# Performance work log

Measured on AMD Instinct MI355X. Metric: run time of the kernel, lower is better.

The kernel has to match this reference:

```python
import jax, jax.numpy as jnp
import numpy as np

EPS = 1.1920929e-07  # torch RMSNorm default eps = float32 finfo eps

def rms_norm(x, w):
    return x * jax.lax.rsqrt(jnp.mean(x * x, axis=-1, keepdims=True) + EPS) * w

def setup_inputs() -> dict:
    key = jax.random.key(0)
    ks = jax.random.split(key, 10)
    B, C, H, W = 8, 64, 48, 48
    E = C  # embed_dim = query_dim = key_dim = value_dim
    q = jax.random.normal(ks[0], (B, C, H, W), jnp.float32)
    k = jax.random.normal(ks[1], (B, C, H, W), jnp.float32)
    v = jax.random.normal(ks[2], (B, C, H, W), jnp.float32)
    s = 1.0 / np.sqrt(E)
    conv_w = jax.random.normal(ks[3], (C, C, 3, 3), jnp.float32) * (1.0 / np.sqrt(C * 9))
    nq_w = jnp.ones((E,), jnp.float32)
    nk_w = jnp.ones((E,), jnp.float32)
    wq = jax.random.normal(ks[4], (E, E), jnp.float32) * s
    bq = jax.random.normal(ks[5], (E,), jnp.float32) * 0.01
    wk = jax.random.normal(ks[6], (E, E), jnp.float32) * s
    bk = jax.random.normal(ks[7], (E,), jnp.float32) * 0.01
    return {"q": q, "k": k, "v": v, "conv_w": conv_w, "nq_w": nq_w,
            "nk_w": nk_w, "wq": wq, "bq": bq, "wk": wk, "bk": bk}

def reference(q, k, v, conv_w, nq_w, nk_w, wq, bq, wk, bk):
    B, C, H, W = q.shape
    num_heads = 4
    head_dim = C // num_heads
    # conv2d 3x3, stride 1, same padding, no bias
    qc = jax.lax.conv_general_dilated(
        q, conv_w, window_strides=(1, 1), padding='SAME',
        dimension_numbers=('NCHW', 'OIHW', 'NCHW'))
    # b c h w -> b (h w) c
    qs = qc.reshape(B, C, H * W).transpose(0, 2, 1)
    ksq = k.reshape(B, C, -1).transpose(0, 2, 1)
    vsq = v.reshape(B, C, -1).transpose(0, 2, 1)
    # RMSNorm on q and k (norm_v output feeds MHA value path whose output is discarded)
    qn = rms_norm(qs, nq_w)
    kn = rms_norm(ksq, nk_w)
    # MHA projections (q scaled by 1/sqrt(head_dim) as in torch)
    qp = (qn @ wq.T + bq) * (1.0 / np.sqrt(head_dim))
    kp = ksq_p = kn @ wk.T + bk
    Sq, Sk = qp.shape[1], kp.shape[1]
    qh = qp.reshape(B, Sq, num_heads, head_dim)
    kh = kp.reshape(B, Sk, num_heads, head_dim)
    scores = jnp.einsum('bihd,bjhd->bhij', qh, kh)
    attn = jax.nn.softmax(scores, axis=-1)
    # average_attn_weights=True -> mean over heads
    attn_avg = jnp.mean(attn, axis=1)  # [b, i, j]
    # custom output: weighted sum over RAW (un-normed, unprojected) value
    out = jnp.einsum('bij,bjd->bid', attn_avg, vsq)
    return out
```

## Files before the change

### kernel.cpp

```cpp
#include <hip/hip_runtime.h>
#include <hip/hip_bf16.h>

namespace {
constexpr int kB = 8;
constexpr int kC = 64;
constexpr int kH = 48;
constexpr int kW = 48;
constexpr int kS = kH * kW;
constexpr float kEps = 1.1920929e-07f;
}

typedef __attribute__((ext_vector_type(8))) short short8;
typedef __attribute__((ext_vector_type(4))) short short4_t;
typedef __attribute__((ext_vector_type(4))) float f32x4;

__device__ __forceinline__ short f2bf(float x) {
  unsigned u = __float_as_uint(x);
  u += 0x7fffu + ((u >> 16) & 1u);
  return (short)(u >> 16);
}
__device__ __forceinline__ float bf2f(short s) {
  return __uint_as_float(((unsigned)(unsigned short)s) << 16);
}

__global__ __launch_bounds__(256) void fused_prep(
    const float* __restrict__ q, const float* __restrict__ k,
    const float* __restrict__ v, const float* __restrict__ wq,
    const float* __restrict__ wk, const float* __restrict__ conv_w,
    short* __restrict__ qt, short* __restrict__ kt, short* __restrict__ vt,
    short* __restrict__ wqb3, short* __restrict__ wkb3, short* __restrict__ wt3) {
  const int blk = blockIdx.x;
  if (blk < 576) {
    __shared__ float tile[64][65];
    const int zz = blk / 36;
    const int bx = blk % 36;
    const int b = zz >> 1;
    const float* src = (zz & 1) ? k : q;
    short* dst = (zz & 1) ? kt : qt;
    const int s0 = bx * 64;
    const int tx = threadIdx.x & 63;
    const int ty = threadIdx.x >> 6;
#pragma unroll
    for (int r = 0; r < 16; ++r) {
      int c = r * 4 + ty;
      tile[c][tx] = src[((size_t)b * kC + c) * kS + s0 + tx];
    }
    __syncthreads();
#pragma unroll
    for (int r = 0; r < 16; ++r) {
      int s = r * 4 + ty;
      dst[((size_t)b * kS + s0 + s) * kC + tx] = f2bf(tile[tx][s]);
    }
  } else if (blk < 1728) {
    int idx = ((blk - 576) * 256 + threadIdx.x) * 4;
    float4 x = *reinterpret_cast<const float4*>(v + idx);
    int2 o;
    o.x = ((int)(unsigned short)f2bf(x.y) << 16) | (unsigned short)f2bf(x.x);
    o.y = ((int)(unsigned short)f2bf(x.w) << 16) | (unsigned short)f2bf(x.z);
    *reinterpret_cast<int2*>(vt + idx) = o;
  } else {
    int idx = (blk - 1728) * 256 + threadIdx.x;
    if (idx < 4096) {
      int j = idx & 7, Lw = (idx >> 3) & 63, slab = idx >> 9;
      int nt = slab & 3, kh = slab >> 2;
      int e = nt * 16 + (Lw & 15), c = kh * 32 + (Lw >> 4) * 8 + j;
      wqb3[idx] = f2bf(wq[e * 64 + c]);
    } else if (idx < 8192) {
      int i2 = idx - 4096;
      int j = i2 & 7, Lw = (i2 >> 3) & 63, slab = i2 >> 9;
      int nt = slab & 3, kh = slab >> 2;
      int e = nt * 16 + (Lw & 15), c = kh * 32 + (Lw >> 4) * 8 + j;
      wkb3[i2] = f2bf(wk[e * 64 + c]);
    } else {
      int i3 = idx - 8192;
      int j = i3 & 7, Lw = (i3 >> 3) & 63, slab = i3 >> 9;
      int nt = slab & 3, kh = (slab >> 2) & 1, tap = slab >> 3;
      int co = nt * 16 + (Lw & 15), ci = kh * 32 + (Lw >> 4) * 8 + j;
      wt3[i3] = f2bf(conv_w[co * 576 + ci * 9 + tap]);
    }
  }
}

__global__ __launch_bounds__(256) void fused_qk_gemm(
    const short* __restrict__ qt, const short* __restrict__ kt,
    const short* __restrict__ wt3, const short* __restrict__ wqb3,
    const short* __restrict__ wkb3,
    const float* __restrict__ nq_w, const float* __restrict__ nk_w,
    const float* __restrict__ bq, const float* __restrict__ bk,
    short* __restrict__ qp, short* __restrict__ kp) {
  __shared__ __align__(16) short Qs[164][72];
  __shared__ __align__(16) short ln[4][16][80];
  const int blk = blockIdx.x;
  const int t = threadIdx.x;
  const int ws = t >> 6;
  const int L = t & 63;
  const int quad = L >> 4;
  const int l16 = L & 15;
  const short8 zero8 = {0, 0, 0, 0, 0, 0, 0, 0};

  if (blk < 288) {
    const int b = blk / 36;
    const int S0 = (blk % 36) * 64;
    const int sBase = S0 + ws * 16;
    const int s = sBase + l16;
    const int h = s / kW, w = s % kW;

    const short* qtb = qt + (size_t)b * kS * kC;
#pragma unroll
    for (int it = 0; it < 6; ++it) {
      int idx = it * 256 + t;
      if (idx < 164 * 8) {
        int r = idx >> 3, sg = idx & 7;
        int srow = S0 - 49 + r;
        srow = srow < 0 ? 0 : (srow >= kS ? kS - 1 : srow);
        *reinterpret_cast<int4*>(&Qs[r][sg * 8]) =
            *reinterpret_cast<const int4*>(qtb + (size_t)srow * kC + sg * 8);
      }
    }
    __syncthreads();

    const int baseLocal = ws * 16 + l16 + 49;
    f32x4 acc[4] = {{0.f, 0.f, 0.f, 0.f}, {0.f, 0.f, 0.f, 0.f},
                    {0.f, 0.f, 0.f, 0.f}, {0.f, 0.f, 0.f, 0.f}};
#pragma unroll
    for (int tap = 0; tap < 9; ++tap) {
      const int dh = tap / 3 - 1, dw = tap % 3 - 1;
      const bool valid = (unsigned)(h + dh) < (unsigned)kH &&
                         (unsigned)(w + dw) < (unsigned)kW;
      const int local = baseLocal + dh * kW + dw;
#pragma unroll
      for (int kh = 0; kh < 2; ++kh) {
        short8 af = *reinterpret_cast<const short8*>(&Qs[local][kh * 32 + quad * 8]);
        af = valid ? af : zero8;
        const short* wb = wt3 + ((tap * 2 + kh) * 4) * 512 + L * 8;
#pragma unroll
        for (int nt = 0; nt < 4; ++nt) {
          short8 bf = *reinterpret_cast<const short8*>(wb + nt * 512);
          acc[nt] = __builtin_amdgcn_mfma_f32_16x16x32_bf16(af, bf, acc[nt], 0, 0, 0);
        }
      }
    }
    float rstd[4];
#pragma unroll
    for (int reg = 0; reg < 4; ++reg) {
      float pr = acc[0][reg] * acc[0][reg] + acc[1][reg] * acc[1][reg]
               + acc[2][reg] * acc[2][reg] + acc[3][reg] * acc[3][reg];
      pr += __shfl_xor(pr, 1, 64);
      pr += __shfl_xor(pr, 2, 64);
      pr += __shfl_xor(pr, 4, 64);
      pr += __shfl_xor(pr, 8, 64);
      rstd[reg] = rsqrtf(pr * (1.0f / kC) + kEps);
    }
#pragma unroll
    for (int nt = 0; nt < 4; ++nt) {
      float g = nq_w[nt * 16 + l16];
#pragma unroll
      for (int reg = 0; reg < 4; ++reg) {
        ln[ws][quad * 4 + reg][nt * 16 + l16] = f2bf(acc[nt][reg] * rstd[reg] * g);
      }
    }
    __syncthreads();
    f32x4 acc2[4] = {{0.f, 0.f, 0.f, 0.f}, {0.f, 0.f, 0.f, 0.f},
                     {0.f, 0.f, 0.f, 0.f}, {0.f, 0.f, 0.f, 0.f}};
#pragma unroll
    for (int kh = 0; kh < 2; ++kh) {
      short8 af = *reinterpret_cast<const short8*>(&ln[ws][l16][kh * 32 + quad * 8]);
      const short* wb = wqb3 + (kh * 4) * 512 + L * 8;
#pragma unroll
      for (int nt = 0; nt < 4; ++nt) {
        short8 bf = *reinterpret_cast<const short8*>(wb + nt * 512);
        acc2[nt] = __builtin_amdgcn_mfma_f32_16x16x32_bf16(af, bf, acc2[nt], 0, 0, 0);
      }
    }
#pragma unroll
    for (int nt = 0; nt < 4; ++nt) {
      const int e = nt * 16 + l16;
      float bias = bq[e];
#pragma unroll
      for (int reg = 0; reg < 4; ++reg) {
        qp[((size_t)b * kS + sBase + quad * 4 + reg) * kC + e] =
            f2bf((acc2[nt][reg] + bias) * 0.25f);
      }
    }
  } else {
    const int idx = blk - 288;
    const int b = idx / 36;
    const int S0 = (idx % 36) * 64;
    const int sBase = S0 + ws * 16;

    const short* ktb = kt + ((size_t)b * kS + S0) * kC;
#pragma unroll
    for (int it = 0; it < 2; ++it) {
      int r = it * 32 + (t >> 3), sg = t & 7;
      *reinterpret_cast<int4*>(&Qs[r][sg * 8]) =
          *reinterpret_cast<const int4*>(ktb + (size_t)r * kC + sg * 8);
    }
    __syncthreads();

    short8 af0 = *reinterpret_cast<const short8*>(&Qs[ws * 16 + l16][quad * 8]);
    short8 af1 = *reinterpret_cast<const short8*>(&Qs[ws * 16 + l16][32 + quad * 8]);

    float xs[16];
#pragma unroll
    for (int j = 0; j < 8; ++j) { xs[j] = bf2f(af0[j]); xs[8 + j] = bf2f(af1[j]); }
    float sum = 0.f;
#pragma unroll
    for (int j = 0; j < 16; ++j) sum = fmaf(xs[j], xs[j], sum);
    sum += __shfl_xor(sum, 16, 64);
    sum += __shfl_xor(sum, 32, 64);
    float rstd = rsqrtf(sum * (1.0f / kC) + kEps);

    const float* n0 = nk_w + quad * 8;
#pragma unroll
    for (int j = 0; j < 8; ++j) {
      af0[j] = f2bf(xs[j] * rstd * n0[j]);
      af1[j] = f2bf(xs[8 + j] * rstd * n0[32 + j]);
    }

    f32x4 acc[4] = {{0.f, 0.f, 0.f, 0.f}, {0.f, 0.f, 0.f, 0.f},
                    {0.f, 0.f, 0.f, 0.f}, {0.f, 0.f, 0.f, 0.f}};
#pragma unroll
    for (int nt = 0; nt < 4; ++nt) {
      short8 bf0 = *reinterpret_cast<const short8*>(
          wkb3 + (0 * 4 + nt) * 512 + L * 8);
      short8 bf1 = *reinterpret_cast<const short8*>(
          wkb3 + (1 * 4 + nt) * 512 + L * 8);
      acc[nt] = __builtin_amdgcn_mfma_f32_16x16x32_bf16(af0, bf0, acc[nt], 0, 0, 0);
      acc[nt] = __builtin_amdgcn_mfma_f32_16x16x32_bf16(af1, bf1, acc[nt], 0, 0, 0);
    }
#pragma unroll
    for (int nt = 0; nt < 4; ++nt) {
      const int e = nt * 16 + l16;
      float bias = bk[e];
#pragma unroll
      for (int reg = 0; reg < 4; ++reg) {
        kp[((size_t)b * kS + sBase + quad * 4 + reg) * kC + e] =
            f2bf(acc[nt][reg] + bias);
      }
    }
  }
}

__global__ __launch_bounds__(256, 3) void attn_flash(
    const short* __restrict__ qp, const short* __restrict__ kp,
    const short* __restrict__ vt, float* __restrict__ out) {
  __shared__ __align__(16) short Kt[2][64][72];
  __shared__ __align__(16) short Vt[2][64][72];
  __shared__ float pl[4][16][4];
  __shared__ float Li[32][4];

  float* slabF = reinterpret_cast<float*>(&Kt[0][0][0]);

  const int blk = blockIdx.x;
  const int b = blk & 7;
  const int i0 = (blk >> 3) * 32;
  const int t = threadIdx.x;
  const int ws = t >> 6;
  const int isub = ws & 1;
  const int jhalf = ws >> 1;
  const int jbase = jhalf * 32;
  const int L = t & 63;
  const int quad = L >> 4;
  const int l16 = L & 15;

  const f32x4 zc = {0.f, 0.f, 0.f, 0.f};
  const short8 z8 = {0, 0, 0, 0, 0, 0, 0, 0};

  const short* qrow = qp + ((size_t)b * kS + i0 + isub * 16 + l16) * kC;
  const short8 qw0 = *reinterpret_cast<const short8*>(qrow + quad * 8);
  const short8 qw1 = *reinterpret_cast<const short8*>(qrow + 32 + quad * 8);
  const bool lo = quad < 2;
  const short8 qm[4] = {lo ? qw0 : z8, lo ? z8 : qw0,
                        lo ? qw1 : z8, lo ? z8 : qw1};

  const int r8i = t >> 3;
  const int seg = t & 7;
  const short* kg = kp + (size_t)b * kS * kC;
  const short* vg = vt + (size_t)b * kC * kS;

  int prow[2];
#pragma unroll
  for (int pass = 0; pass < 2; ++pass) {
    int jo = pass * 32 + r8i;
    int p32 = jo & 31;
    prow[pass] = (jo & 32) | ((p32 & 4) << 2) | (((p32 >> 3) & 3) << 2) | (p32 & 3);
  }

  int4 kreg[2], vreg[2];
#pragma unroll
  for (int pass = 0; pass < 2; ++pass) {
    kreg[pass] = *reinterpret_cast<const int4*>(
        kg + (size_t)(pass * 32 + r8i) * kC + seg * 8);
    vreg[pass] = *reinterpret_cast<const int4*>(
        vg + (size_t)(pass * 32 + r8i) * kS + seg * 8);
  }
#pragma unroll
  for (int pass = 0; pass < 2; ++pass) {
    *reinterpret_cast<int4*>(&Kt[0][prow[pass]][seg * 8]) = kreg[pass];
    *reinterpret_cast<int4*>(&Vt[0][pass * 32 + r8i][seg * 8]) = vreg[pass];
  }
  __syncthreads();

  f32x4 U[4][4];
#pragma unroll
  for (int h = 0; h < 4; ++h)
#pragma unroll
    for (int d = 0; d < 4; ++d) U[h][d] = zc;
  float lh[4] = {0.f, 0.f, 0.f, 0.f};

  for (int jt = 0; jt < kS / 64; ++jt) {
    const int buf = jt & 1;
    const bool more = (jt + 1) < kS / 64;
    if (more) {
      const int jn = (jt + 1) * 64;
#pragma unroll
      for (int pass = 0; pass < 2; ++pass) {
        kreg[pass] = *reinterpret_cast<const int4*>(
            kg + (size_t)(jn + pass * 32 + r8i) * kC + seg * 8);
        vreg[pass] = *reinterpret_cast<const int4*>(
            vg + (size_t)(pass * 32 + r8i) * kS + jn + seg * 8);
      }
    }

    short8 kf[2][2];
#pragma unroll
    for (int c = 0; c < 2; ++c)
#pragma unroll
      for (int w = 0; w < 2; ++w)
        kf[c][w] = *reinterpret_cast<const short8*>(
            &Kt[buf][jbase + c * 16 + l16][w * 32 + quad * 8]);
    short8 vf[4];
#pragma unroll
    for (int d = 0; d < 4; ++d)
      vf[d] = *reinterpret_cast<const short8*>(
          &Vt[buf][d * 16 + l16][jbase + quad * 8]);

#pragma unroll
    for (int h = 0; h < 4; ++h) {
      const int w = h >> 1;
      f32x4 s0 = __builtin_amdgcn_mfma_f32_16x16x32_bf16(kf[0][w], qm[h], zc, 0, 0, 0);
      f32x4 s1 = __builtin_amdgcn_mfma_f32_16x16x32_bf16(kf[1][w], qm[h], zc, 0, 0, 0);
      float e0 = __expf(s0[0]), e1 = __expf(s0[1]);
      float e2 = __expf(s0[2]), e3 = __expf(s0[3]);
      float f0 = __expf(s1[0]), f1 = __expf(s1[1]);
      float f2 = __expf(s1[2]), f3 = __expf(s1[3]);
      lh[h] += ((e0 + e1) + (e2 + e3)) + ((f0 + f1) + (f2 + f3));
      union { __hip_bfloat162 h2[4]; short8 s8; } cv;
      cv.h2[0] = __float22bfloat162_rn(make_float2(e0, e1));
      cv.h2[1] = __float22bfloat162_rn(make_float2(e2, e3));
      cv.h2[2] = __float22bfloat162_rn(make_float2(f0, f1));
      cv.h2[3] = __float22bfloat162_rn(make_float2(f2, f3));
#pragma unroll
      for (int d = 0; d < 4; ++d)
        U[h][d] = __builtin_amdgcn_mfma_f32_16x16x32_bf16(vf[d], cv.s8, U[h][d], 0, 0, 0);
    }

    if (more) {
      const int nb = buf ^ 1;
#pragma unroll
      for (int pass = 0; pass < 2; ++pass) {
        *reinterpret_cast<int4*>(&Kt[nb][prow[pass]][seg * 8]) = kreg[pass];
        *reinterpret_cast<int4*>(&Vt[nb][pass * 32 + r8i][seg * 8]) = vreg[pass];
      }
    }
    __syncthreads();
  }

#pragma unroll
  for (int h = 0; h < 4; ++h) {
    lh[h] += __shfl_xor(lh[h], 16, 64);
    lh[h] += __shfl_xor(lh[h], 32, 64);
  }
  if (quad == 0) {
#pragma unroll
    for (int h = 0; h < 4; ++h) pl[ws][l16][h] = lh[h];
  }
  __syncthreads();
  if (t < 128) {
    const int i = t >> 2, h = t & 3;
    Li[i][h] = 0.25f / (pl[i >> 4][i & 15][h] + pl[(i >> 4) + 2][i & 15][h]);
  }
  __syncthreads();
  float c[4];
#pragma unroll
  for (int h = 0; h < 4; ++h) c[h] = Li[isub * 16 + l16][h];

#pragma unroll
  for (int d = 0; d < 4; ++d) {
    if (jhalf == 1) {
#pragma unroll
      for (int h = 0; h < 4; ++h)
#pragma unroll
        for (int reg = 0; reg < 4; ++reg)
          slabF[((isub * 4 + h) * 4 + reg) * 66 + L] = U[h][d][reg];
    }
    __syncthreads();
    if (jhalf == 0) {
      float of[4] = {0.f, 0.f, 0.f, 0.f};
#pragma unroll
      for (int h = 0; h < 4; ++h) {
#pragma unroll
        for (int reg = 0; reg < 4; ++reg) {
          float tot = U[h][d][reg] + slabF[((isub * 4 + h) * 4 + reg) * 66 + L];
          of[reg] += tot * c[h];
        }
      }
      *reinterpret_cast<float4*>(
          out + ((size_t)b * kS + i0 + isub * 16 + l16) * kC + d * 16 + quad * 4) =
          make_float4(of[0], of[1], of[2], of[3]);
    }
    __syncthreads();
  }
}

extern "C" void kernel_launch(void* const* d_in, const int* in_sizes, int n_in,
                              void* d_out, int out_size, void* d_ws, size_t ws_size,
                              hipStream_t stream) {
  const float* q      = (const float*)d_in[0];
  const float* k      = (const float*)d_in[1];
  const float* v      = (const float*)d_in[2];
  const float* conv_w = (const float*)d_in[3];
  const float* nq_w   = (const float*)d_in[4];
  const float* nk_w   = (const float*)d_in[5];
  const float* wq     = (const float*)d_in[6];
  const float* bq     = (const float*)d_in[7];
  const float* wk     = (const float*)d_in[8];
  const float* bk     = (const float*)d_in[9];
  float* out = (float*)d_out;

  const size_t N = (size_t)kB * kS * kC;
  short* qt   = (short*)d_ws;
  short* kt   = qt + N;
  short* vt   = kt + N;
  short* qp   = vt + N;
  short* kp   = qp + N;
  short* wqb3 = kp + N;
  short* wkb3 = wqb3 + 4096;
  short* wt3  = wkb3 + 4096;

  fused_prep<<<1904, 256, 0, stream>>>(q, k, v, wq, wk, conv_w,
                                       qt, kt, vt, wqb3, wkb3, wt3);
  fused_qk_gemm<<<576, 256, 0, stream>>>(qt, kt, wt3, wqb3, wkb3,
                                         nq_w, nk_w, bq, bk, qp, kp);
  attn_flash<<<576, 256, 0, stream>>>(qp, kp, vt, out);
}
```

Measured before the change: 154.0 us.

## Split attention heads across blocks with atomic output and exp2 softmax

The attention kernel now splits the four heads into two pairs, one per block, which doubles the grid to 1152 blocks. Each block loads only half of K, and the two partial outputs are combined with atomicAdd into an output that is zeroed by a memset first. The log2(e) factor is folded into the q scale so the softmax can use the hardware exp2 directly, and launch bounds are raised to allow more resident blocks. In exchange, the V tile is loaded and the PV MFMAs are done twice (once per head pair), and the atomics plus the extra memset add traffic.

```diff
diff --git a/kernel.cpp b/kernel.cpp
--- a/kernel.cpp
+++ b/kernel.cpp
@@ -8,10 +8,10 @@
 constexpr int kW = 48;
 constexpr int kS = kH * kW;
 constexpr float kEps = 1.1920929e-07f;
+constexpr float kQScale = 0.25f * 1.4426950408889634f;
 }
 
 typedef __attribute__((ext_vector_type(8))) short short8;
-typedef __attribute__((ext_vector_type(4))) short short4_t;
 typedef __attribute__((ext_vector_type(4))) float f32x4;
 
 __device__ __forceinline__ short f2bf(float x) {
@@ -21,6 +21,9 @@
 }
 __device__ __forceinline__ float bf2f(short s) {
   return __uint_as_float(((unsigned)(unsigned short)s) << 16);
+}
+__device__ __forceinline__ float fexp2(float x) {
+  return __builtin_amdgcn_exp2f(x);
 }
 
 __global__ __launch_bounds__(256) void fused_prep(
@@ -179,7 +182,7 @@
 #pragma unroll
       for (int reg = 0; reg < 4; ++reg) {
         qp[((size_t)b * kS + sBase + quad * 4 + reg) * kC + e] =
-            f2bf((acc2[nt][reg] + bias) * 0.25f);
+            f2bf((acc2[nt][reg] + bias) * kQScale);
       }
     }
   } else {
@@ -241,19 +244,21 @@
   }
 }
 
-__global__ __launch_bounds__(256, 3) void attn_flash(
+__global__ __launch_bounds__(256, 5) void attn_flash(
     const short* __restrict__ qp, const short* __restrict__ kp,
     const short* __restrict__ vt, float* __restrict__ out) {
-  __shared__ __align__(16) short Kt[2][64][72];
+  __shared__ __align__(16) short Kt[2][64][40];
   __shared__ __align__(16) short Vt[2][64][72];
-  __shared__ float pl[4][16][4];
-  __shared__ float Li[32][4];
+  __shared__ float pl[4][16][2];
+  __shared__ float Li[32][2];
 
   float* slabF = reinterpret_cast<float*>(&Kt[0][0][0]);
 
   const int blk = blockIdx.x;
   const int b = blk & 7;
-  const int i0 = (blk >> 3) * 32;
+  const int idx = blk >> 3;
+  const int hp = idx & 1;
+  const int i0 = (idx >> 1) * 32;
   const int t = threadIdx.x;
   const int ws = t >> 6;
   const int isub = ws & 1;
@@ -266,69 +271,59 @@
   const f32x4 zc = {0.f, 0.f, 0.f, 0.f};
   const short8 z8 = {0, 0, 0, 0, 0, 0, 0, 0};
 
-  const short* qrow = qp + ((size_t)b * kS + i0 + isub * 16 + l16) * kC;
-  const short8 qw0 = *reinterpret_cast<const short8*>(qrow + quad * 8);
-  const short8 qw1 = *reinterpret_cast<const short8*>(qrow + 32 + quad * 8);
+  const short* qrow = qp + ((size_t)b * kS + i0 + isub * 16 + l16) * kC + hp * 32;
+  const short8 qw = *reinterpret_cast<const short8*>(qrow + quad * 8);
   const bool lo = quad < 2;
-  const short8 qm[4] = {lo ? qw0 : z8, lo ? z8 : qw0,
-                        lo ? qw1 : z8, lo ? z8 : qw1};
-
+  const short8 qm[2] = {lo ? qw : z8, lo ? z8 : qw};
+
+  const int rK = t >> 2;
+  const int segK = t & 3;
   const int r8i = t >> 3;
   const int seg = t & 7;
-  const short* kg = kp + (size_t)b * kS * kC;
+  const short* kg = kp + (size_t)b * kS * kC + hp * 32;
   const short* vg = vt + (size_t)b * kC * kS;
 
-  int prow[2];
-#pragma unroll
-  for (int pass = 0; pass < 2; ++pass) {
-    int jo = pass * 32 + r8i;
-    int p32 = jo & 31;
-    prow[pass] = (jo & 32) | ((p32 & 4) << 2) | (((p32 >> 3) & 3) << 2) | (p32 & 3);
-  }
-
-  int4 kreg[2], vreg[2];
-#pragma unroll
-  for (int pass = 0; pass < 2; ++pass) {
-    kreg[pass] = *reinterpret_cast<const int4*>(
-        kg + (size_t)(pass * 32 + r8i) * kC + seg * 8);
+  const int p32 = rK & 31;
+  const int prowK =
+      (rK & 32) | ((p32 & 4) << 2) | (((p32 >> 3) & 3) << 2) | (p32 & 3);
+
+  int4 kreg, vreg[2];
+  kreg = *reinterpret_cast<const int4*>(kg + (size_t)rK * kC + segK * 8);
+#pragma unroll
+  for (int pass = 0; pass < 2; ++pass)
     vreg[pass] = *reinterpret_cast<const int4*>(
         vg + (size_t)(pass * 32 + r8i) * kS + seg * 8);
-  }
-#pragma unroll
-  for (int pass = 0; pass < 2; ++pass) {
-    *reinterpret_cast<int4*>(&Kt[0][prow[pass]][seg * 8]) = kreg[pass];
+  *reinterpret_cast<int4*>(&Kt[0][prowK][segK * 8]) = kreg;
+#pragma unroll
+  for (int pass = 0; pass < 2; ++pass)
     *reinterpret_cast<int4*>(&Vt[0][pass * 32 + r8i][seg * 8]) = vreg[pass];
-  }
   __syncthreads();
 
-  f32x4 U[4][4];
-#pragma unroll
-  for (int h = 0; h < 4; ++h)
-#pragma unroll
-    for (int d = 0; d < 4; ++d) U[h][d] = zc;
-  float lh[4] = {0.f, 0.f, 0.f, 0.f};
+  f32x4 U[2][4];
+#pragma unroll
+  for (int hl = 0; hl < 2; ++hl)
+#pragma unroll
+    for (int d = 0; d < 4; ++d) U[hl][d] = zc;
+  float lh[2] = {0.f, 0.f};
 
   for (int jt = 0; jt < kS / 64; ++jt) {
     const int buf = jt & 1;
     const bool more = (jt + 1) < kS / 64;
     if (more) {
       const int jn = (jt + 1) * 64;
-#pragma unroll
-      for (int pass = 0; pass < 2; ++pass) {
-        kreg[pass] = *reinterpret_cast<const int4*>(
-            kg + (size_t)(jn + pass * 32 + r8i) * kC + seg * 8);
+      kreg = *reinterpret_cast<const int4*>(
+          kg + (size_t)(jn + rK) * kC + segK * 8);
+#pragma unroll
+      for (int pass = 0; pass < 2; ++pass)
         vreg[pass] = *reinterpret_cast<const int4*>(
             vg + (size_t)(pass * 32 + r8i) * kS + jn + seg * 8);
-      }
-    }
-
-    short8 kf[2][2];
+    }
+
+    short8 kf[2];
 #pragma unroll
     for (int c = 0; c < 2; ++c)
-#pragma unroll
-      for (int w = 0; w < 2; ++w)
-        kf[c][w] = *reinterpret_cast<const short8*>(
-            &Kt[buf][jbase + c * 16 + l16][w * 32 + quad * 8]);
+      kf[c] = *reinterpret_cast<const short8*>(
+          &Kt[buf][jbase + c * 16 + l16][quad * 8]);
     short8 vf[4];
 #pragma unroll
     for (int d = 0; d < 4; ++d)
@@ -336,15 +331,14 @@
           &Vt[buf][d * 16 + l16][jbase + quad * 8]);
 
 #pragma unroll
-    for (int h = 0; h < 4; ++h) {
-      const int w = h >> 1;
-      f32x4 s0 = __builtin_amdgcn_mfma_f32_16x16x32_bf16(kf[0][w], qm[h], zc, 0, 0, 0);
-      f32x4 s1 = __builtin_amdgcn_mfma_f32_16x16x32_bf16(kf[1][w], qm[h], zc, 0, 0, 0);
-      float e0 = __expf(s0[0]), e1 = __expf(s0[1]);
-      float e2 = __expf(s0[2]), e3 = __expf(s0[3]);
-      float f0 = __expf(s1[0]), f1 = __expf(s1[1]);
-      float f2 = __expf(s1[2]), f3 = __expf(s1[3]);
-      lh[h] += ((e0 + e1) + (e2 + e3)) + ((f0 + f1) + (f2 + f3));
+    for (int hl = 0; hl < 2; ++hl) {
+      f32x4 s0 = __builtin_amdgcn_mfma_f32_16x16x32_bf16(kf[0], qm[hl], zc, 0, 0, 0);
+      f32x4 s1 = __builtin_amdgcn_mfma_f32_16x16x32_bf16(kf[1], qm[hl], zc, 0, 0, 0);
+      float e0 = fexp2(s0[0]), e1 = fexp2(s0[1]);
+      float e2 = fexp2(s0[2]), e3 = fexp2(s0[3]);
+      float f0 = fexp2(s1[0]), f1 = fexp2(s1[1]);
+      float f2 = fexp2(s1[2]), f3 = fexp2(s1[3]);
+      lh[hl] += ((e0 + e1) + (e2 + e3)) + ((f0 + f1) + (f2 + f3));
       union { __hip_bfloat162 h2[4]; short8 s8; } cv;
       cv.h2[0] = __float22bfloat162_rn(make_float2(e0, e1));
       cv.h2[1] = __float22bfloat162_rn(make_float2(e2, e3));
@@ -352,62 +346,61 @@
       cv.h2[3] = __float22bfloat162_rn(make_float2(f2, f3));
 #pragma unroll
       for (int d = 0; d < 4; ++d)
-        U[h][d] = __builtin_amdgcn_mfma_f32_16x16x32_bf16(vf[d], cv.s8, U[h][d], 0, 0, 0);
+        U[hl][d] = __builtin_amdgcn_mfma_f32_16x16x32_bf16(vf[d], cv.s8, U[hl][d], 0, 0, 0);
     }
 
     if (more) {
       const int nb = buf ^ 1;
-#pragma unroll
-      for (int pass = 0; pass < 2; ++pass) {
-        *reinterpret_cast<int4*>(&Kt[nb][prow[pass]][seg * 8]) = kreg[pass];
+      *reinterpret_cast<int4*>(&Kt[nb][prowK][segK * 8]) = kreg;
+#pragma unroll
+      for (int pass = 0; pass < 2; ++pass)
         *reinterpret_cast<int4*>(&Vt[nb][pass * 32 + r8i][seg * 8]) = vreg[pass];
-      }
-    }
-    __syncthreads();
-  }
-
-#pragma unroll
-  for (int h = 0; h < 4; ++h) {
-    lh[h] += __shfl_xor(lh[h], 16, 64);
-    lh[h] += __shfl_xor(lh[h], 32, 64);
+    }
+    __syncthreads();
+  }
+
+#pragma unroll
+  for (int hl = 0; hl < 2; ++hl) {
+    lh[hl] += __shfl_xor(lh[hl], 16, 64);
+    lh[hl] += __shfl_xor(lh[hl], 32, 64);
   }
   if (quad == 0) {
 #pragma unroll
-    for (int h = 0; h < 4; ++h) pl[ws][l16][h] = lh[h];
+    for (int hl = 0; hl < 2; ++hl) pl[ws][l16][hl] = lh[hl];
   }
   __syncthreads();
-  if (t < 128) {
-    const int i = t >> 2, h = t & 3;
-    Li[i][h] = 0.25f / (pl[i >> 4][i & 15][h] + pl[(i >> 4) + 2][i & 15][h]);
+  if (t < 64) {
+    const int i = t >> 1, h2 = t & 1;
+    Li[i][h2] = 0.25f / (pl[i >> 4][i & 15][h2] + pl[(i >> 4) + 2][i & 15][h2]);
   }
   __syncthreads();
-  float c[4];
-#pragma unroll
-  for (int h = 0; h < 4; ++h) c[h] = Li[isub * 16 + l16][h];
+  float c2[2];
+#pragma unroll
+  for (int hl = 0; hl < 2; ++hl) c2[hl] = Li[isub * 16 + l16][hl];
 
 #pragma unroll
   for (int d = 0; d < 4; ++d) {
     if (jhalf == 1) {
 #pragma unroll
-      for (int h = 0; h < 4; ++h)
+      for (int hl = 0; hl < 2; ++hl)
 #pragma unroll
         for (int reg = 0; reg < 4; ++reg)
-          slabF[((isub * 4 + h) * 4 + reg) * 66 + L] = U[h][d][reg];
+          slabF[((isub * 2 + hl) * 4 + reg) * 66 + L] = U[hl][d][reg];
     }
     __syncthreads();
     if (jhalf == 0) {
       float of[4] = {0.f, 0.f, 0.f, 0.f};
 #pragma unroll
-      for (int h = 0; h < 4; ++h) {
+      for (int hl = 0; hl < 2; ++hl) {
 #pragma unroll
         for (int reg = 0; reg < 4; ++reg) {
-          float tot = U[h][d][reg] + slabF[((isub * 4 + h) * 4 + reg) * 66 + L];
-          of[reg] += tot * c[h];
+          float tot = U[hl][d][reg] + slabF[((isub * 2 + hl) * 4 + reg) * 66 + L];
+          of[reg] += tot * c2[hl];
         }
       }
-      *reinterpret_cast<float4*>(
-          out + ((size_t)b * kS + i0 + isub * 16 + l16) * kC + d * 16 + quad * 4) =
-          make_float4(of[0], of[1], of[2], of[3]);
+      float* op = out + ((size_t)b * kS + i0 + isub * 16 + l16) * kC + d * 16 + quad * 4;
+#pragma unroll
+      for (int reg = 0; reg < 4; ++reg) atomicAdd(op + reg, of[reg]);
     }
     __syncthreads();
   }
@@ -438,9 +431,11 @@
   short* wkb3 = wqb3 + 4096;
   short* wt3  = wkb3 + 4096;
 
+  hipMemsetAsync(d_out, 0, out_size, stream);
+
   fused_prep<<<1904, 256, 0, stream>>>(q, k, v, wq, wk, conv_w,
                                        qt, kt, vt, wqb3, wkb3, wt3);
   fused_qk_gemm<<<576, 256, 0, stream>>>(qt, kt, wt3, wqb3, wkb3,
                                          nq_w, nk_w, bq, bk, qp, kp);
-  attn_flash<<<576, 256, 0, stream>>>(qp, kp, vt, out);
-}
+  attn_flash<<<1152, 256, 0, stream>>>(qp, kp, vt, out);
+}
```

Measured after the change: 155.4 us. No clear change (+0.9%).
